# Kernel tuning notes

Hardware: AMD Instinct MI355X
Metric: run time of the kernel (lower is better)

## Reference

```python
import jax, jax.numpy as jnp
import numpy as np

E = 16           # num_experts
D = 4096         # hidden_size
F = 688          # per-expert SwiGLU intermediate size
N = 8192         # total tokens (bsz*seq_len)
CAP_FACTOR = 1.25


def setup_inputs() -> dict:
    key = jax.random.key(0)
    k1, k2, k3, k4, k5, k6 = jax.random.split(key, 6)
    return {
        "x": jax.random.normal(k1, (N, D), dtype=jnp.float32),
        "topk_idx": jax.random.randint(k2, (N,), 0, E, dtype=jnp.int32),
        "topk_scores": jax.random.uniform(k3, (N,), dtype=jnp.float32),
        "Wg": jax.random.normal(k4, (E, D, F), dtype=jnp.float32) * 0.02,
        "Wu": jax.random.normal(k5, (E, D, F), dtype=jnp.float32) * 0.02,
        "Wd": jax.random.normal(k6, (E, F, D), dtype=jnp.float32) * 0.02,
    }


def reference(x, topk_idx, topk_scores, Wg, Wu, Wd):
    # Switch-style top-1 MoE with capacity-based token dropping.
    # Deterministic variant: tokens beyond capacity are dropped in token order
    # (original uses randperm; the math pattern is identical).
    n, d = x.shape
    e = Wg.shape[0]
    cap = int(CAP_FACTOR * n / e)  # static under jit

    # position of each token within its assigned expert (0-based)
    oh = jax.nn.one_hot(topk_idx, e, dtype=jnp.int32)            # [N, E]
    pos = jnp.take_along_axis(jnp.cumsum(oh, axis=0) - 1,
                              topk_idx[:, None].astype(jnp.int32), axis=1)[:, 0]
    keep = pos < cap                                             # [N] bool

    # dispatch: scatter kept tokens into [E, cap, D]; dropped go to dummy row E
    e_safe = jnp.where(keep, topk_idx, e)
    p_safe = jnp.minimum(pos, cap - 1)
    buf = jnp.zeros((e + 1, cap, d), x.dtype).at[e_safe, p_safe].set(x)[:e]

    # per-expert SwiGLU FFN: down(silu(gate(x)) * up(x))
    h = jax.nn.silu(jnp.einsum('ecd,edf->ecf', buf, Wg)) \
        * jnp.einsum('ecd,edf->ecf', buf, Wu)                    # [E, cap, F]
    out = jnp.einsum('ecf,efd->ecd', h, Wd)                      # [E, cap, D]

    # combine: gather back, zero-pad dropped tokens, scale by gate scores
    y = out[topk_idx, p_safe] * keep[:, None].astype(x.dtype)
    y = y * topk_scores[:, None]
    return y
```

## Files before the change

kernel.cpp:

```cpp
#include <hip/hip_runtime.h>
#include <hip/hip_bf16.h>

#define E_ 16
#define D_ 4096
#define F_ 688
#define N_ 8192
#define CAP_ 640
#define NFT_ 11
#define NKT32_ 128
#define NFT32_ 22

typedef __attribute__((ext_vector_type(8))) short bf16x8;
typedef __attribute__((ext_vector_type(4))) float f32x4;
typedef __attribute__((ext_vector_type(4))) float fvec4;
typedef __attribute__((ext_vector_type(4))) unsigned short usvec4;
typedef __attribute__((ext_vector_type(8))) unsigned short usvec8;

__device__ __forceinline__ unsigned short f2bf(float f) {
    __hip_bfloat16 h = __float2bfloat16(f);
    return __builtin_bit_cast(unsigned short, h);
}
__device__ __forceinline__ void gload16(const unsigned short* g, unsigned short* l) {
    __builtin_amdgcn_global_load_lds(
        (const __attribute__((address_space(1))) unsigned int*)g,
        (__attribute__((address_space(3))) unsigned int*)l, 16, 0, 0);
}

#define WAITV(N) asm volatile("s_waitcnt vmcnt(" #N ")" ::: "memory")
#define SBAR     __builtin_amdgcn_s_barrier()
#define SCHED0   __builtin_amdgcn_sched_barrier(0)


__global__ void k_dispatch(const int* __restrict__ idx,
                           int* __restrict__ slot_token,
                           int* __restrict__ row_of,
                           int* __restrict__ cnt) {
    __shared__ int hist[256][E_];
    const int t = threadIdx.x;
#pragma unroll
    for (int e = 0; e < E_; e++) hist[t][e] = 0;
    __syncthreads();
    const int base = t * (N_ / 256);
    for (int j = 0; j < N_ / 256; j++) {
        int e = idx[base + j];
        hist[t][e]++;
    }
    __syncthreads();
    if (t < E_) {
        int run = 0;
        for (int i = 0; i < 256; i++) { int v = hist[i][t]; hist[i][t] = run; run += v; }
        cnt[t] = run < CAP_ ? run : CAP_;
    }
    for (int s = t; s < E_ * CAP_; s += 256) slot_token[s] = -1;
    __syncthreads();
    for (int j = 0; j < N_ / 256; j++) {
        int i = base + j;
        int e = idx[i];
        int p = hist[t][e]++;
        if (p < CAP_) { slot_token[e * CAP_ + p] = i; row_of[i] = e * CAP_ + p; }
        else          { row_of[i] = -1; }
    }
}

__global__ void k_zero_dropped(const int* __restrict__ row_of, float* __restrict__ y) {
    for (int i = blockIdx.x; i < N_; i += gridDim.x) {
        if (row_of[i] >= 0) continue;
        fvec4* yp = (fvec4*)(y + (size_t)i * D_);
        fvec4 z = {0.f, 0.f, 0.f, 0.f};
        for (int c = threadIdx.x; c < D_ / 4; c += 256) yp[c] = z;
    }
}

__global__ void k_gather(const float* __restrict__ x, const int* __restrict__ slot_token,
                         unsigned short* __restrict__ Aimg) {
    const int strip = blockIdx.y;
    const int kg = blockIdx.x;
    const int t = threadIdx.x;
    const int r = t >> 1, h = t & 1;
    const int tok = slot_token[strip * 128 + r];
#pragma unroll
    for (int i = 0; i < 8; i++) {
        const int kt = kg * 8 + i;
        unsigned short* dst = Aimg + ((size_t)strip * NKT32_ + kt) * 4096;
        usvec8 p0, p1;
        if (tok < 0) {
            usvec8 z = {0, 0, 0, 0, 0, 0, 0, 0};
            p0 = z; p1 = z;
        } else {
            const float* src = x + (size_t)tok * D_ + kt * 32 + h * 16;
            fvec4 a = *(const fvec4*)(src);
            fvec4 b = *(const fvec4*)(src + 4);
            fvec4 c = *(const fvec4*)(src + 8);
            fvec4 d = *(const fvec4*)(src + 12);
            usvec8 q0 = {f2bf(a[0]), f2bf(a[1]), f2bf(a[2]), f2bf(a[3]),
                         f2bf(b[0]), f2bf(b[1]), f2bf(b[2]), f2bf(b[3])};
            usvec8 q1 = {f2bf(c[0]), f2bf(c[1]), f2bf(c[2]), f2bf(c[3]),
                         f2bf(d[0]), f2bf(d[1]), f2bf(d[2]), f2bf(d[3])};
            p0 = q0; p1 = q1;
        }
        *(usvec8*)&dst[(2 * h) * 1024 + r * 8]     = p0;
        *(usvec8*)&dst[(2 * h + 1) * 1024 + r * 8] = p1;
    }
}

__global__ void k_wprep_gu(const float* __restrict__ Wg, const float* __restrict__ Wu,
                           unsigned short* __restrict__ img) {
    const int ft = blockIdx.x, kt = blockIdx.y, e = blockIdx.z;
    const int tid = threadIdx.x;
    const int f4 = (tid & 15) * 4, kq4 = (tid >> 4) * 4;
    const int gf = ft * 64 + f4;
    const bool v = gf < F_;
    const fvec4 fz = {0.f, 0.f, 0.f, 0.f};
    fvec4 g[4], u[4];
#pragma unroll
    for (int r = 0; r < 4; r++) {
        size_t off = (size_t)e * D_ * F_ + (size_t)(kt * 64 + kq4 + r) * F_ + gf;
        g[r] = v ? *(const fvec4*)(Wg + off) : fz;
        u[r] = v ? *(const fvec4*)(Wu + off) : fz;
    }
    const int t32 = kq4 >> 5, kl = kq4 & 31;
    unsigned short* dst = img + ((size_t)(e * NKT32_ + kt * 2 + t32) * NFT_ + ft) * 4096;
    const int ubase = (kl >> 3) * 512 + (kl & 7);
#pragma unroll
    for (int i = 0; i < 4; i++) {
        usvec4 pg = {f2bf(g[0][i]), f2bf(g[1][i]), f2bf(g[2][i]), f2bf(g[3][i])};
        usvec4 pu = {f2bf(u[0][i]), f2bf(u[1][i]), f2bf(u[2][i]), f2bf(u[3][i])};
        *(usvec4*)&dst[ubase + (f4 + i) * 8]        = pg;
        *(usvec4*)&dst[2048 + ubase + (f4 + i) * 8] = pu;
    }
}

__global__ void k_wprep_d(const float* __restrict__ Wd, unsigned short* __restrict__ img) {
    const int dt = blockIdx.x, kt = blockIdx.y, e = blockIdx.z;
    const int tid = threadIdx.x;
    const int d4 = (tid & 15) * 4, kq4 = (tid >> 4) * 4;
    const int gd = dt * 64 + d4;
    const fvec4 fz = {0.f, 0.f, 0.f, 0.f};
    fvec4 b[4];
#pragma unroll
    for (int r = 0; r < 4; r++) {
        int krow = kt * 64 + kq4 + r;
        b[r] = (krow < F_) ? *(const fvec4*)(Wd + (size_t)e * F_ * D_ + (size_t)krow * D_ + gd) : fz;
    }
    const int t32 = kq4 >> 5, kl = kq4 & 31;
    unsigned short* dst = img + ((size_t)(e * NFT32_ + kt * 2 + t32) * 64 + dt) * 2048;
    const int ubase = (kl >> 3) * 512 + (kl & 7);
#pragma unroll
    for (int i = 0; i < 4; i++) {
        usvec4 p = {f2bf(b[0][i]), f2bf(b[1][i]), f2bf(b[2][i]), f2bf(b[3][i])};
        *(usvec4*)&dst[ubase + (d4 + i) * 8] = p;
    }
}

__global__ __launch_bounds__(256, 3) void k_gemm1_dma(
    const unsigned short* __restrict__ Aimg, const unsigned short* __restrict__ Wgu,
    const int* __restrict__ cnt, unsigned short* __restrict__ Himg) {
    const int bid = blockIdx.x;
    const int xcd = bid & 7;
    const int j = bid >> 3;
    const int mb = j % 5;
    const int gl = j / 5;
    const int group = xcd * 22 + gl;
    const int e = group / NFT_, fidx = group % NFT_;
    const int m0 = mb * 128;
    if (m0 >= cnt[e]) return;
    const int strip = e * 5 + mb;

    __shared__ __align__(16) unsigned short As[3][4096];
    __shared__ __align__(16) unsigned short Bgu[3][4096];

    const int tid = threadIdx.x;
    const int lane = tid & 63, wave = tid >> 6;
    const int wm = wave >> 1, wn = wave & 1;
    const int wq = wave * 1024;

    f32x4 accG[4][2], accU[4][2];
#pragma unroll
    for (int a = 0; a < 4; a++)
#pragma unroll
        for (int b = 0; b < 2; b++) {
            f32x4 z = {0.f, 0.f, 0.f, 0.f};
            accG[a][b] = z; accU[a][b] = z;
        }

    const unsigned short* Astrip = Aimg + (size_t)strip * NKT32_ * 4096;
    const unsigned short* WguE = Wgu + ((size_t)e * NKT32_ * NFT_ + fidx) * 4096;

#define G1STAGE(T, BUF)                                                        \
    {                                                                          \
        const unsigned short* asrc = Astrip + (size_t)(T) * 4096 + wq;         \
        gload16(asrc + lane * 8,       &As[BUF][wq]);                          \
        gload16(asrc + 512 + lane * 8, &As[BUF][wq + 512]);                    \
        const unsigned short* bsrc = WguE + (size_t)(T) * (NFT_ * 4096) + wq;  \
        gload16(bsrc + lane * 8,       &Bgu[BUF][wq]);                         \
        gload16(bsrc + 512 + lane * 8, &Bgu[BUF][wq + 512]);                   \
    }

    G1STAGE(0, 0)
    G1STAGE(1, 1)
    WAITV(4);
    SBAR;

    const int arow8 = (wm * 64 + (lane & 15)) * 8;
    const int brow8 = (wn * 32 + (lane & 15)) * 8;
    const int kg = lane >> 4;

    for (int kt = 0; kt < NKT32_; ++kt) {
        const int cur = kt % 3;
        if (kt + 2 < NKT32_) G1STAGE(kt + 2, (kt + 2) % 3)
        SCHED0;
        __builtin_amdgcn_s_setprio(1);
        {
            bf16x8 av[4], bgv[2], buv[2];
#pragma unroll
            for (int mi = 0; mi < 4; mi++)
                av[mi] = *(const bf16x8*)&As[cur][kg * 1024 + arow8 + mi * 128];
#pragma unroll
            for (int ni = 0; ni < 2; ni++) {
                bgv[ni] = *(const bf16x8*)&Bgu[cur][kg * 512 + brow8 + ni * 128];
                buv[ni] = *(const bf16x8*)&Bgu[cur][2048 + kg * 512 + brow8 + ni * 128];
            }
#pragma unroll
            for (int mi = 0; mi < 4; mi++)
#pragma unroll
                for (int ni = 0; ni < 2; ni++) {
                    accG[mi][ni] = __builtin_amdgcn_mfma_f32_16x16x32_bf16(av[mi], bgv[ni], accG[mi][ni], 0, 0, 0);
                    accU[mi][ni] = __builtin_amdgcn_mfma_f32_16x16x32_bf16(av[mi], buv[ni], accU[mi][ni], 0, 0, 0);
                }
        }
        __builtin_amdgcn_s_setprio(0);
        SCHED0;
        if (kt + 2 < NKT32_) WAITV(4); else WAITV(0);
        if (kt + 1 < NKT32_) SBAR;
    }
#undef G1STAGE

    unsigned short* Hs = Himg + (size_t)(strip * NFT32_ + fidx * 2) * 4096;
#pragma unroll
    for (int mi = 0; mi < 4; mi++)
#pragma unroll
        for (int ni = 0; ni < 2; ni++) {
            int fl = wn * 32 + ni * 16 + (lane & 15);
            int rl = wm * 64 + mi * 16 + ((lane >> 4) << 2);
            unsigned short* Ht = Hs + (size_t)(fl >> 5) * 4096 + ((fl & 31) >> 3) * 1024 + (fl & 7);
#pragma unroll
            for (int q = 0; q < 4; q++) {
                float g = accG[mi][ni][q], u = accU[mi][ni][q];
                float h = g * u / (1.f + __expf(-g));
                Ht[(rl + q) * 8] = f2bf(h);
            }
        }
}

__global__ __launch_bounds__(256, 4) void k_gemm2_dma(
    const unsigned short* __restrict__ Himg, const unsigned short* __restrict__ WdI,
    const int* __restrict__ slot_token, const int* __restrict__ cnt,
    const float* __restrict__ scores, float* __restrict__ y) {
    const int bid = blockIdx.x;
    const int xcd = bid & 7;
    const int j = bid >> 3;
    const int mb = j % 5;
    const int gl = j / 5;
    const int group = xcd * 128 + gl;
    const int e = group >> 6, didx = group & 63;
    const int m0 = mb * 128, d0 = didx * 64;
    if (m0 >= cnt[e]) return;
    const int strip = e * 5 + mb;

    __shared__ __align__(16) unsigned short As[3][4096];
    __shared__ __align__(16) unsigned short Bd[3][2048];
    __shared__ int tokS[128];
    __shared__ float scS[128];

    const int tid = threadIdx.x;
    const int lane = tid & 63, wave = tid >> 6;
    const int wm = wave >> 1, wn = wave & 1;
    const int wq = wave * 1024;

    if (tid < 128) {
        int t = slot_token[e * CAP_ + m0 + tid];
        tokS[tid] = t;
        scS[tid] = (t >= 0) ? scores[t] : 0.f;
    }
    __syncthreads();

    f32x4 acc[4][2];
#pragma unroll
    for (int a = 0; a < 4; a++)
#pragma unroll
        for (int b = 0; b < 2; b++) {
            f32x4 z = {0.f, 0.f, 0.f, 0.f};
            acc[a][b] = z;
        }

    const unsigned short* Hstrip = Himg + (size_t)strip * NFT32_ * 4096;
    const unsigned short* WdE = WdI + ((size_t)e * NFT32_ * 64 + didx) * 2048;

#define G2STAGE(T, BUF)                                                        \
    {                                                                          \
        const unsigned short* asrc = Hstrip + (size_t)(T) * 4096 + wq;         \
        gload16(asrc + lane * 8,       &As[BUF][wq]);                          \
        gload16(asrc + 512 + lane * 8, &As[BUF][wq + 512]);                    \
        const unsigned short* bsrc = WdE + (size_t)(T) * (64 * 2048) + wave * 512; \
        gload16(bsrc + lane * 8, &Bd[BUF][wave * 512]);                        \
    }

    G2STAGE(0, 0)
    G2STAGE(1, 1)
    WAITV(3);
    SBAR;

    const int arow8 = (wm * 64 + (lane & 15)) * 8;
    const int brow8 = (wn * 32 + (lane & 15)) * 8;
    const int kg = lane >> 4;

    for (int fc = 0; fc < NFT32_; ++fc) {
        const int cur = fc % 3;
        if (fc + 2 < NFT32_) G2STAGE(fc + 2, (fc + 2) % 3)
        SCHED0;
        __builtin_amdgcn_s_setprio(1);
        {
            bf16x8 av[4], bv[2];
#pragma unroll
            for (int mi = 0; mi < 4; mi++)
                av[mi] = *(const bf16x8*)&As[cur][kg * 1024 + arow8 + mi * 128];
#pragma unroll
            for (int ni = 0; ni < 2; ni++)
                bv[ni] = *(const bf16x8*)&Bd[cur][kg * 512 + brow8 + ni * 128];
#pragma unroll
            for (int mi = 0; mi < 4; mi++)
#pragma unroll
                for (int ni = 0; ni < 2; ni++)
                    acc[mi][ni] = __builtin_amdgcn_mfma_f32_16x16x32_bf16(av[mi], bv[ni], acc[mi][ni], 0, 0, 0);
        }
        __builtin_amdgcn_s_setprio(0);
        SCHED0;
        if (fc + 2 < NFT32_) WAITV(3); else WAITV(0);
        if (fc + 1 < NFT32_) SBAR;
    }
#undef G2STAGE

#pragma unroll
    for (int mi = 0; mi < 4; mi++)
#pragma unroll
        for (int ni = 0; ni < 2; ni++) {
            int d = d0 + wn * 32 + ni * 16 + (lane & 15);
            int rowb = wm * 64 + mi * 16 + ((lane >> 4) << 2);
#pragma unroll
            for (int q = 0; q < 4; q++) {
                int row = rowb + q;
                int t = tokS[row];
                if (t >= 0) y[(size_t)t * D_ + d] = acc[mi][ni][q] * scS[row];
            }
        }
}

extern "C" void kernel_launch(void* const* d_in, const int* in_sizes, int n_in,
                              void* d_out, int out_size, void* d_ws, size_t ws_size,
                              hipStream_t stream) {
    const float* x   = (const float*)d_in[0];
    const int*   idx = (const int*)d_in[1];
    const float* sc  = (const float*)d_in[2];
    const float* Wg  = (const float*)d_in[3];
    const float* Wu  = (const float*)d_in[4];
    const float* Wd  = (const float*)d_in[5];
    float* y = (float*)d_out;

    char* ws = (char*)d_ws;
    int* slot_token = (int*)ws;
    int* row_of     = (int*)(ws + 40960);
    int* cnt        = (int*)(ws + 40960 + 32768);
    const size_t hoff   = 131072;
    const size_t hbytes = (size_t)80 * NFT32_ * 8192;
    unsigned short* Himg = (unsigned short*)(ws + hoff);
    const size_t aoff   = hoff + hbytes;
    const size_t abytes = (size_t)80 * NKT32_ * 8192;
    unsigned short* Aimg = (unsigned short*)(ws + aoff);
    const size_t guoff   = aoff + abytes;
    const size_t gubytes = (size_t)E_ * NKT32_ * NFT_ * 8192;
    unsigned short* WguI = (unsigned short*)(ws + guoff);
    const size_t wdoff   = guoff + gubytes;
    unsigned short* WdI  = (unsigned short*)(ws + wdoff);

    k_dispatch<<<1, 256, 0, stream>>>(idx, slot_token, row_of, cnt);
    k_zero_dropped<<<128, 256, 0, stream>>>(row_of, y);
    k_gather<<<dim3(16, 80), 256, 0, stream>>>(x, slot_token, Aimg);
    k_wprep_gu<<<dim3(NFT_, 64, E_), 256, 0, stream>>>(Wg, Wu, WguI);
    k_wprep_d<<<dim3(64, NFT_, E_), 256, 0, stream>>>(Wd, WdI);
    k_gemm1_dma<<<880, 256, 0, stream>>>(Aimg, WguI, cnt, Himg);
    k_gemm2_dma<<<5120, 256, 0, stream>>>(Himg, WdI, slot_token, cnt, sc, y);
}
```

Measured before the change: 591.2 us.

## Load A operand directly into registers and double K-step per pipeline stage

Both GEMM kernels stop staging the activation (A) tile through LDS. Each wave now loads its A fragments straight from global memory into a double-buffered register set, while the weight (B) tiles still go to LDS through a triple-buffered async DMA that now covers two K-chunks per stage. This halves the number of barriers and removes the LDS traffic for A, at the cost of more VGPRs and vmcnt accounting that depends on hand-counted outstanding loads. The second kernel's occupancy hint drops from 4 to 3 to leave room for the larger register footprint.

```diff
diff --git a/kernel.cpp b/kernel.cpp
--- a/kernel.cpp
+++ b/kernel.cpp
@@ -26,9 +26,9 @@
         (__attribute__((address_space(3))) unsigned int*)l, 16, 0, 0);
 }
 
-#define WAITV(N) asm volatile("s_waitcnt vmcnt(" #N ")" ::: "memory")
-#define SBAR     __builtin_amdgcn_s_barrier()
-#define SCHED0   __builtin_amdgcn_sched_barrier(0)
+#define WAITVN(N) asm volatile("s_waitcnt vmcnt(" #N ")" ::: "memory")
+#define SBAR      __builtin_amdgcn_s_barrier()
+#define SCHED0    __builtin_amdgcn_sched_barrier(0)
 
 
 __global__ void k_dispatch(const int* __restrict__ idx,
@@ -166,8 +166,7 @@
     if (m0 >= cnt[e]) return;
     const int strip = e * 5 + mb;
 
-    __shared__ __align__(16) unsigned short As[3][4096];
-    __shared__ __align__(16) unsigned short Bgu[3][4096];
+    __shared__ __align__(16) unsigned short Bgu[3][8192];
 
     const int tid = threadIdx.x;
     const int lane = tid & 63, wave = tid >> 6;
@@ -185,55 +184,73 @@
 
     const unsigned short* Astrip = Aimg + (size_t)strip * NKT32_ * 4096;
     const unsigned short* WguE = Wgu + ((size_t)e * NKT32_ * NFT_ + fidx) * 4096;
-
-#define G1STAGE(T, BUF)                                                        \
-    {                                                                          \
-        const unsigned short* asrc = Astrip + (size_t)(T) * 4096 + wq;         \
-        gload16(asrc + lane * 8,       &As[BUF][wq]);                          \
-        gload16(asrc + 512 + lane * 8, &As[BUF][wq + 512]);                    \
-        const unsigned short* bsrc = WguE + (size_t)(T) * (NFT_ * 4096) + wq;  \
-        gload16(bsrc + lane * 8,       &Bgu[BUF][wq]);                         \
-        gload16(bsrc + 512 + lane * 8, &Bgu[BUF][wq + 512]);                   \
-    }
-
-    G1STAGE(0, 0)
-    G1STAGE(1, 1)
-    WAITV(4);
-    SBAR;
-
-    const int arow8 = (wm * 64 + (lane & 15)) * 8;
-    const int brow8 = (wn * 32 + (lane & 15)) * 8;
-    const int kg = lane >> 4;
-
-    for (int kt = 0; kt < NKT32_; ++kt) {
-        const int cur = kt % 3;
-        if (kt + 2 < NKT32_) G1STAGE(kt + 2, (kt + 2) % 3)
-        SCHED0;
-        __builtin_amdgcn_s_setprio(1);
-        {
-            bf16x8 av[4], bgv[2], buv[2];
-#pragma unroll
-            for (int mi = 0; mi < 4; mi++)
-                av[mi] = *(const bf16x8*)&As[cur][kg * 1024 + arow8 + mi * 128];
-#pragma unroll
-            for (int ni = 0; ni < 2; ni++) {
-                bgv[ni] = *(const bf16x8*)&Bgu[cur][kg * 512 + brow8 + ni * 128];
-                buv[ni] = *(const bf16x8*)&Bgu[cur][2048 + kg * 512 + brow8 + ni * 128];
-            }
-#pragma unroll
-            for (int mi = 0; mi < 4; mi++)
-#pragma unroll
-                for (int ni = 0; ni < 2; ni++) {
-                    accG[mi][ni] = __builtin_amdgcn_mfma_f32_16x16x32_bf16(av[mi], bgv[ni], accG[mi][ni], 0, 0, 0);
-                    accU[mi][ni] = __builtin_amdgcn_mfma_f32_16x16x32_bf16(av[mi], buv[ni], accU[mi][ni], 0, 0, 0);
-                }
-        }
-        __builtin_amdgcn_s_setprio(0);
-        SCHED0;
-        if (kt + 2 < NKT32_) WAITV(4); else WAITV(0);
-        if (kt + 1 < NKT32_) SBAR;
-    }
-#undef G1STAGE
+    const int GUS = NFT_ * 4096;
+    const int afo = (lane >> 4) * 1024 + (wm * 64 + (lane & 15)) * 8;
+    const int bfo = (lane >> 4) * 512 + (wn * 32 + (lane & 15)) * 8;
+
+    bf16x8 a0[8], a1[8];
+
+#define LOADA1(T, S)                                                             \
+    {                                                                            \
+        const unsigned short* ab = Astrip + (size_t)(2 * (T)) * 4096 + afo;      \
+        _Pragma("unroll") for (int mi = 0; mi < 4; mi++) {                       \
+            S[mi]     = *(const bf16x8*)(ab + mi * 128);                         \
+            S[mi + 4] = *(const bf16x8*)(ab + 4096 + mi * 128);                  \
+        }                                                                        \
+    }
+#define DMAB1(T, BUF)                                                            \
+    {                                                                            \
+        const unsigned short* b0 = WguE + (size_t)(2 * (T)) * GUS + wq;          \
+        gload16(b0 + lane * 8,       &Bgu[BUF][wq]);                             \
+        gload16(b0 + 512 + lane * 8, &Bgu[BUF][wq + 512]);                       \
+        const unsigned short* b1 = b0 + GUS;                                     \
+        gload16(b1 + lane * 8,       &Bgu[BUF][4096 + wq]);                      \
+        gload16(b1 + 512 + lane * 8, &Bgu[BUF][4096 + wq + 512]);                \
+    }
+#define MFMAS1(BUF, S)                                                           \
+    {                                                                            \
+        __builtin_amdgcn_s_setprio(1);                                           \
+        _Pragma("unroll") for (int kh = 0; kh < 2; kh++) {                       \
+            bf16x8 bg[2], bu[2];                                                 \
+            _Pragma("unroll") for (int ni = 0; ni < 2; ni++) {                   \
+                bg[ni] = *(const bf16x8*)&Bgu[BUF][kh * 4096 + bfo + ni * 128];  \
+                bu[ni] = *(const bf16x8*)&Bgu[BUF][kh * 4096 + 2048 + bfo + ni * 128]; \
+            }                                                                    \
+            _Pragma("unroll") for (int mi = 0; mi < 4; mi++)                     \
+            _Pragma("unroll") for (int ni = 0; ni < 2; ni++) {                   \
+                accG[mi][ni] = __builtin_amdgcn_mfma_f32_16x16x32_bf16(S[kh * 4 + mi], bg[ni], accG[mi][ni], 0, 0, 0); \
+                accU[mi][ni] = __builtin_amdgcn_mfma_f32_16x16x32_bf16(S[kh * 4 + mi], bu[ni], accU[mi][ni], 0, 0, 0); \
+            }                                                                    \
+        }                                                                        \
+        __builtin_amdgcn_s_setprio(0);                                           \
+    }
+#define G1IT(T, CS, NS, WN)                                                      \
+    {                                                                            \
+        SBAR;                                                                    \
+        if ((T) + 1 < 64) { LOADA1((T) + 1, NS) }                                \
+        if ((T) + 2 < 64) { const int nb_ = ((T) + 2) % 3; DMAB1((T) + 2, nb_) } \
+        SCHED0;                                                                  \
+        WAITVN(WN);                                                              \
+        SCHED0;                                                                  \
+        { const int cb_ = (T) % 3; MFMAS1(cb_, CS) }                             \
+    }
+
+    LOADA1(0, a0)
+    SCHED0;
+    DMAB1(0, 0)
+    DMAB1(1, 1)
+    SCHED0;
+
+    for (int m = 0; m < 31; m++) {
+        G1IT(2 * m,     a0, a1, 16)
+        G1IT(2 * m + 1, a1, a0, 16)
+    }
+    G1IT(62, a0, a1, 12)
+    G1IT(63, a1, a0, 0)
+#undef G1IT
+#undef MFMAS1
+#undef DMAB1
+#undef LOADA1
 
     unsigned short* Hs = Himg + (size_t)(strip * NFT32_ + fidx * 2) * 4096;
 #pragma unroll
@@ -252,7 +269,7 @@
         }
 }
 
-__global__ __launch_bounds__(256, 4) void k_gemm2_dma(
+__global__ __launch_bounds__(256, 3) void k_gemm2_dma(
     const unsigned short* __restrict__ Himg, const unsigned short* __restrict__ WdI,
     const int* __restrict__ slot_token, const int* __restrict__ cnt,
     const float* __restrict__ scores, float* __restrict__ y) {
@@ -267,15 +284,13 @@
     if (m0 >= cnt[e]) return;
     const int strip = e * 5 + mb;
 
-    __shared__ __align__(16) unsigned short As[3][4096];
-    __shared__ __align__(16) unsigned short Bd[3][2048];
+    __shared__ __align__(16) unsigned short Bd[3][4096];
     __shared__ int tokS[128];
     __shared__ float scS[128];
 
     const int tid = threadIdx.x;
     const int lane = tid & 63, wave = tid >> 6;
     const int wm = wave >> 1, wn = wave & 1;
-    const int wq = wave * 1024;
 
     if (tid < 128) {
         int t = slot_token[e * CAP_ + m0 + tid];
@@ -295,50 +310,71 @@
 
     const unsigned short* Hstrip = Himg + (size_t)strip * NFT32_ * 4096;
     const unsigned short* WdE = WdI + ((size_t)e * NFT32_ * 64 + didx) * 2048;
-
-#define G2STAGE(T, BUF)                                                        \
-    {                                                                          \
-        const unsigned short* asrc = Hstrip + (size_t)(T) * 4096 + wq;         \
-        gload16(asrc + lane * 8,       &As[BUF][wq]);                          \
-        gload16(asrc + 512 + lane * 8, &As[BUF][wq + 512]);                    \
-        const unsigned short* bsrc = WdE + (size_t)(T) * (64 * 2048) + wave * 512; \
-        gload16(bsrc + lane * 8, &Bd[BUF][wave * 512]);                        \
-    }
-
-    G2STAGE(0, 0)
-    G2STAGE(1, 1)
-    WAITV(3);
-    SBAR;
-
-    const int arow8 = (wm * 64 + (lane & 15)) * 8;
-    const int brow8 = (wn * 32 + (lane & 15)) * 8;
-    const int kg = lane >> 4;
-
-    for (int fc = 0; fc < NFT32_; ++fc) {
-        const int cur = fc % 3;
-        if (fc + 2 < NFT32_) G2STAGE(fc + 2, (fc + 2) % 3)
-        SCHED0;
-        __builtin_amdgcn_s_setprio(1);
-        {
-            bf16x8 av[4], bv[2];
-#pragma unroll
-            for (int mi = 0; mi < 4; mi++)
-                av[mi] = *(const bf16x8*)&As[cur][kg * 1024 + arow8 + mi * 128];
-#pragma unroll
-            for (int ni = 0; ni < 2; ni++)
-                bv[ni] = *(const bf16x8*)&Bd[cur][kg * 512 + brow8 + ni * 128];
-#pragma unroll
-            for (int mi = 0; mi < 4; mi++)
-#pragma unroll
-                for (int ni = 0; ni < 2; ni++)
-                    acc[mi][ni] = __builtin_amdgcn_mfma_f32_16x16x32_bf16(av[mi], bv[ni], acc[mi][ni], 0, 0, 0);
-        }
-        __builtin_amdgcn_s_setprio(0);
-        SCHED0;
-        if (fc + 2 < NFT32_) WAITV(3); else WAITV(0);
-        if (fc + 1 < NFT32_) SBAR;
-    }
-#undef G2STAGE
+    const int WDS = 64 * 2048;
+    const int afo = (lane >> 4) * 1024 + (wm * 64 + (lane & 15)) * 8;
+    const int bfo = (lane >> 4) * 512 + (wn * 32 + (lane & 15)) * 8;
+
+    bf16x8 a0[8], a1[8];
+
+#define LOADA2(T, S)                                                             \
+    {                                                                            \
+        const unsigned short* ab = Hstrip + (size_t)(2 * (T)) * 4096 + afo;      \
+        _Pragma("unroll") for (int mi = 0; mi < 4; mi++) {                       \
+            S[mi]     = *(const bf16x8*)(ab + mi * 128);                         \
+            S[mi + 4] = *(const bf16x8*)(ab + 4096 + mi * 128);                  \
+        }                                                                        \
+    }
+#define DMAB2(T, BUF)                                                            \
+    {                                                                            \
+        const unsigned short* b0 = WdE + (size_t)(2 * (T)) * WDS + wave * 512;   \
+        gload16(b0 + lane * 8,       &Bd[BUF][wave * 512]);                      \
+        gload16(b0 + WDS + lane * 8, &Bd[BUF][2048 + wave * 512]);               \
+    }
+#define MFMAS2(BUF, S)                                                           \
+    {                                                                            \
+        __builtin_amdgcn_s_setprio(1);                                           \
+        _Pragma("unroll") for (int kh = 0; kh < 2; kh++) {                       \
+            bf16x8 bv[2];                                                        \
+            _Pragma("unroll") for (int ni = 0; ni < 2; ni++)                     \
+                bv[ni] = *(const bf16x8*)&Bd[BUF][kh * 2048 + bfo + ni * 128];   \
+            _Pragma("unroll") for (int mi = 0; mi < 4; mi++)                     \
+            _Pragma("unroll") for (int ni = 0; ni < 2; ni++)                     \
+                acc[mi][ni] = __builtin_amdgcn_mfma_f32_16x16x32_bf16(S[kh * 4 + mi], bv[ni], acc[mi][ni], 0, 0, 0); \
+        }                                                                        \
+        __builtin_amdgcn_s_setprio(0);                                           \
+    }
+#define G2IT(T, CS, NS, WN)                                                      \
+    {                                                                            \
+        SBAR;                                                                    \
+        if ((T) + 1 < 11) { LOADA2((T) + 1, NS) }                                \
+        if ((T) + 2 < 11) { const int nb_ = ((T) + 2) % 3; DMAB2((T) + 2, nb_) } \
+        SCHED0;                                                                  \
+        WAITVN(WN);                                                              \
+        SCHED0;                                                                  \
+        { const int cb_ = (T) % 3; MFMAS2(cb_, CS) }                             \
+    }
+
+    LOADA2(0, a0)
+    SCHED0;
+    DMAB2(0, 0)
+    DMAB2(1, 1)
+    SCHED0;
+
+    G2IT(0, a0, a1, 12)
+    G2IT(1, a1, a0, 12)
+    G2IT(2, a0, a1, 12)
+    G2IT(3, a1, a0, 12)
+    G2IT(4, a0, a1, 12)
+    G2IT(5, a1, a0, 12)
+    G2IT(6, a0, a1, 12)
+    G2IT(7, a1, a0, 12)
+    G2IT(8, a0, a1, 12)
+    G2IT(9, a1, a0, 10)
+    G2IT(10, a0, a1, 0)
+#undef G2IT
+#undef MFMAS2
+#undef DMAB2
+#undef LOADA2
 
 #pragma unroll
     for (int mi = 0; mi < 4; mi++)
```

New measurement: 518.5 us. 12.3% less time.
